# Optimization experiments

Measured on AMD Instinct MI355X. Metric: run time of the kernel, lower is better.

The kernel has to match this reference:

```python
import jax, jax.numpy as jnp
import numpy as np

jax.config.update("jax_enable_x64", True)  # original uses double for Cholesky stability

LAM = 1.0


def _safe_pow(x, a):
    # |x|**a, with a gradient-safe handling of x == 0 (result is 0 for a > 0;
    # naive 0**a has nan grad w.r.t. a via log(0)).
    ax = jnp.abs(x)
    safe = jnp.where(ax == 0, 1.0, ax)
    return jnp.where(ax == 0, 0.0, safe ** a)


def _dx_cov(alpha, tau, T):
    # fGn (increment) covariance; stationary -> depends only on lag k = j - i (Toeplitz)
    t = jnp.arange(T - 1, dtype=jnp.float64)
    DT = (t[None, :] - t[:, None])[None, :, :]          # [1, T-1, T-1]
    a = alpha[:, None, None].astype(jnp.float64)        # [BS, 1, 1]
    tb = tau[:, None, None].astype(jnp.float64)
    R = 0.5 * (_safe_pow(DT + 1.0, a) + _safe_pow(DT - 1.0, a) - 2.0 * _safe_pow(DT, a))
    adt = jnp.abs(DT)
    # exponential taper beyond lag tau; clamp exponent so unused branch can't overflow
    decay = jnp.exp(-LAM * jnp.maximum(adt - tb, 0.0))
    R = jnp.where(adt >= tb, R * decay, R)
    return R                                            # [BS, T-1, T-1] float64


def setup_inputs() -> dict:
    key = jax.random.key(0)
    k1, k2, k3, k4 = jax.random.split(key, 4)
    BS, T, dim = 64, 1024, 3
    alpha = (0.5 + jax.random.uniform(k1, (BS,))).astype(jnp.float32)        # (0.5, 1.5) valid fBM exponent
    tau = (20.0 + 50.0 * jax.random.uniform(k2, (BS,))).astype(jnp.float32)  # taper lag > 0
    diffusion = (0.5 + jax.random.uniform(k3, (BS,))).astype(jnp.float32)
    du = jax.random.normal(k4, (BS, T - 1, dim), dtype=jnp.float32)          # hoisted torch.randn
    return {"alpha": alpha, "tau": tau, "diffusion": diffusion, "du": du, "T": T}


def reference(alpha, tau, diffusion, du, T):
    BS, dim = alpha.shape[0], du.shape[-1]
    C = _dx_cov(alpha, tau, T)                           # [BS, T-1, T-1] float64
    L = jnp.linalg.cholesky(C).astype(jnp.float32)       # batched Cholesky, cast like torch
    du_s = du * jnp.sqrt(diffusion)[:, None, None]       # scale noise by sqrt(D)
    dx = L @ du_s                                        # [BS, T-1, dim]
    x = jnp.cumsum(dx, axis=1)
    zeros = jnp.zeros((BS, 1, dim), dtype=x.dtype)
    return jnp.concatenate([zeros, x], axis=1)           # [BS, T, dim]
```

## Files before the change

### kernel.cpp

```cpp
#include <hip/hip_runtime.h>
#include <math.h>


#define TM1 1023
#define NTH 1024
#define K0  128
#define CSTRIDE 129

__device__ __forceinline__ float bperm(int a, float v) {
    return __int_as_float(__builtin_amdgcn_ds_bpermute(a, __float_as_int(v)));
}
__device__ __forceinline__ float rdlane(float v, int s) {
    return __int_as_float(__builtin_amdgcn_readlane(__float_as_int(v), s));
}
__device__ __forceinline__ float dpp_shl1(float v) {
    return __int_as_float(__builtin_amdgcn_update_dpp(
        0, __float_as_int(v), 0x130, 0xF, 0xF, true));
}
__device__ __forceinline__ int uslot(int k) { return ((k & 3) << 8) | (k >> 2); }

__device__ __forceinline__ float4 ldus(const float4* us4s, int k) {
    int kc = (k < 0) ? 0 : k;
    float4 v = us4s[uslot(kc)];
    if (k < 0) { v.x = 0.f; v.y = 0.f; v.z = 0.f; }
    return v;
}

template<bool MIXED>
__device__ __forceinline__ void conv_quad(
    const float4* us4s, const float* colDT, float lca, float lcb,
    int B, int jq, int quad, float4* ypx4, float4* ypy4, float4* ypz4)
{
    const int   j0   = jq << 5;
    const float lsel = (jq < 2) ? lca : lcb;

    float4 q0 = MIXED ? ldus(us4s, B + 0 - j0) : us4s[uslot(B + 0 - j0)];
    float4 q1 = MIXED ? ldus(us4s, B + 1 - j0) : us4s[uslot(B + 1 - j0)];
    float4 q2 = MIXED ? ldus(us4s, B + 2 - j0) : us4s[uslot(B + 2 - j0)];
    float4 q3 = MIXED ? ldus(us4s, B + 3 - j0) : us4s[uslot(B + 3 - j0)];

    float a0x=0,a0y=0,a0z=0, a1x=0,a1y=0,a1z=0;
    float a2x=0,a2y=0,a2z=0, a3x=0,a3y=0,a3z=0;

    #pragma unroll 8
    for (int jj = 0; jj < 32; ++jj) {
        const int j = j0 + jj;
        float lcj = rdlane(lsel, j & 63);
        float c0 = lcj, c1 = lcj, c2 = lcj, c3 = lcj;
        if (MIXED) {
            int p = B - j;
            float4 h = *reinterpret_cast<const float4*>(&colDT[(j << 7) + B]);
            c0 = (p + 0 < 128) ? h.x : lcj;
            c1 = (p + 1 < 128) ? h.y : lcj;
            c2 = (p + 2 < 128) ? h.z : lcj;
            c3 = (p + 3 < 128) ? h.w : lcj;
        }
        a0x = fmaf(c0, q0.x, a0x); a0y = fmaf(c0, q0.y, a0y); a0z = fmaf(c0, q0.z, a0z);
        a1x = fmaf(c1, q1.x, a1x); a1y = fmaf(c1, q1.y, a1y); a1z = fmaf(c1, q1.z, a1z);
        a2x = fmaf(c2, q2.x, a2x); a2y = fmaf(c2, q2.y, a2y); a2z = fmaf(c2, q2.z, a2z);
        a3x = fmaf(c3, q3.x, a3x); a3y = fmaf(c3, q3.y, a3y); a3z = fmaf(c3, q3.z, a3z);
        int xi = B - j - 1;
        float4 nv = MIXED ? ldus(us4s, xi) : us4s[uslot(xi)];
        q3 = q2; q2 = q1; q1 = q0; q0 = nv;
    }
    ypx4[(jq << 8) + quad] = make_float4(a0x, a1x, a2x, a3x);
    ypy4[(jq << 8) + quad] = make_float4(a0y, a1y, a2y, a3y);
    ypz4[(jq << 8) + quad] = make_float4(a0z, a1z, a2z, a3z);
}

__global__ __launch_bounds__(NTH, 1)
void fbm_schur_kernel(const float* __restrict__ alpha,
                      const float* __restrict__ tau,
                      const float* __restrict__ diffusion,
                      const float* __restrict__ du,
                      float* __restrict__ out)
{
    const int b   = blockIdx.x;
    const int tid = threadIdx.x;
    const int w   = tid >> 6;
    const int l   = tid & 63;

    __shared__ float  colDT[K0 * CSTRIDE];
    __shared__ float4 us4[1024];
    __shared__ float4 ypx4[4 * 256];
    __shared__ float4 ypy4[4 * 256];
    __shared__ float4 ypz4[4 * 256];
    __shared__ float  Lc[128];
    __shared__ float  wtot[48];

    const float sd = sqrtf(diffusion[b]);
    const float* dub = du + (size_t)b * (TM1 * 3);

    if (w > 0) {
        for (int e = tid - 64; e < TM1 * 3; e += (NTH - 64)) {
            int k = e / 3, d = e - 3 * k;
            ((float*)&us4[uslot(k)])[d] = dub[e] * sd;
        }
        for (int i = tid - 64; i < K0; i += (NTH - 64))
            colDT[i * CSTRIDE + 128] = 0.f;
        if (tid == 64) us4[uslot(1023)] = make_float4(0.f, 0.f, 0.f, 0.f);
    } else {
        const double a  = (double)alpha[b];
        const double tb = (double)tau[b];
        auto cov = [&](int k) -> float {
            if (k == 0) return 1.0f;
            double dk = (double)k;
            double ck = 0.5 * (pow(dk + 1.0, a) + pow(dk - 1.0, a) - 2.0 * pow(dk, a));
            if (dk >= tb) ck *= exp(tb - dk);
            return (float)ck;
        };
        float g1a = cov(l);
        float g1b = cov(l + 64);
        float g2a = (l == 0) ? 0.f : g1a;
        float g2b = g1b;

        int probe = __builtin_amdgcn_update_dpp(0, l + 100, 0x130, 0xF, 0xF, true);
        const bool dpp_ok = (__builtin_amdgcn_readlane(probe, 5) == 106);
        const int addr_up = ((l + 1) & 63) << 2;

#define SCHUR_LOOP(SHA, SHB)                                               \
        for (int k = 0; k < K0; ++k) {                                     \
            float den  = rdlane(g1a, 0);                                   \
            float sc   = __frsqrt_rn(den);                                 \
            colDT[l * CSTRIDE + k]        = g1a * sc;                      \
            colDT[(64 + l) * CSTRIDE + k] = g1b * sc;                      \
            float num  = rdlane(g2a, 1);                                   \
            float r    = num * __builtin_amdgcn_rcpf(den);                 \
            float wrap = rdlane(g2b, 0);                                   \
            float g2pa = (SHA);                                            \
            float g2pb = (SHB);                                            \
            if (l == 63) { g2pa = wrap; g2pb = 0.f; }                      \
            float n1a = fmaf(-r, g2pa, g1a);                               \
            float n1b = fmaf(-r, g2pb, g1b);                               \
            g2a = fmaf(-r, g1a, g2pa);                                     \
            g2b = fmaf(-r, g1b, g2pb);                                     \
            g1a = n1a; g1b = n1b;                                          \
        }
        if (dpp_ok) {
            SCHUR_LOOP(dpp_shl1(g2a), dpp_shl1(g2b))
        } else {
            SCHUR_LOOP(bperm(addr_up, g2a), bperm(addr_up, g2b))
        }
#undef SCHUR_LOOP
        float sc = __frsqrt_rn(rdlane(g1a, 0));
        Lc[l]      = g1a * sc;
        Lc[64 + l] = g1b * sc;
    }
    __syncthreads();

    {
        float lca = Lc[l], lcb = Lc[64 + l];
        const int jq   = w & 3;
        const int rb   = w >> 2;
        const int quad = (rb << 6) + l;
        const int B    = quad << 2;
        if (rb == 0)
            conv_quad<true >(us4, colDT, lca, lcb, B, jq, quad, ypx4, ypy4, ypz4);
        else
            conv_quad<false>(us4, colDT, lca, lcb, B, jq, quad, ypx4, ypy4, ypz4);
    }
    __syncthreads();

    const int i = tid;
    float sx = 0.f, sy = 0.f, sz = 0.f;
    if (i < TM1) {
        const float* px = (const float*)ypx4;
        const float* py = (const float*)ypy4;
        const float* pz = (const float*)ypz4;
        sx = px[i] + px[1024 + i] + px[2048 + i] + px[3072 + i];
        sy = py[i] + py[1024 + i] + py[2048 + i] + py[3072 + i];
        sz = pz[i] + pz[1024 + i] + pz[2048 + i] + pz[3072 + i];
    }
    #pragma unroll
    for (int off = 1; off < 64; off <<= 1) {
        float tx = __shfl_up(sx, off);
        float ty = __shfl_up(sy, off);
        float tz = __shfl_up(sz, off);
        if (l >= off) { sx += tx; sy += ty; sz += tz; }
    }
    if (l == 63) { wtot[w * 3 + 0] = sx; wtot[w * 3 + 1] = sy; wtot[w * 3 + 2] = sz; }
    __syncthreads();

    float ox = 0.f, oy = 0.f, oz = 0.f;
    for (int q = 0; q < w; ++q) {
        ox += wtot[q * 3 + 0]; oy += wtot[q * 3 + 1]; oz += wtot[q * 3 + 2];
    }
    float* outb = out + (size_t)b * (TM1 + 1) * 3;
    if (i < TM1) {
        outb[(i + 1) * 3 + 0] = sx + ox;
        outb[(i + 1) * 3 + 1] = sy + oy;
        outb[(i + 1) * 3 + 2] = sz + oz;
    }
    if (tid == 0) { outb[0] = 0.f; outb[1] = 0.f; outb[2] = 0.f; }
}

extern "C" void kernel_launch(void* const* d_in, const int* in_sizes, int n_in,
                              void* d_out, int out_size, void* d_ws, size_t ws_size,
                              hipStream_t stream)
{
    const float* alpha     = (const float*)d_in[0];
    const float* tau       = (const float*)d_in[1];
    const float* diffusion = (const float*)d_in[2];
    const float* du        = (const float*)d_in[3];
    float* out = (float*)d_out;
    const int BS = in_sizes[0];

    fbm_schur_kernel<<<dim3(BS), dim3(NTH), 0, stream>>>(
        alpha, tau, diffusion, du, out);
}
```

Before: 76.50 us.

## Truncate Schur recursion by tau, reuse pow values, track pivot, DPP scan

Limits the Schur/Levinson recursion to K = min(128, ceil(tau)+48) steps, relying on the exponential taper so later columns equal the stationary limit column. Cuts the number of double pow calls by computing one pow per lag and sharing neighbours through shuffles. Updates the pivot algebraically instead of reading it with readlane, which shortens the serial dependency chain. Replaces the shuffle-based wave prefix scan with a DPP scan guarded by a runtime check. Truncating at K is an approximation whose accuracy depends on tau and the 48-lag margin.

```diff
diff --git a/kernel.cpp b/kernel.cpp
--- a/kernel.cpp
+++ b/kernel.cpp
@@ -16,6 +16,21 @@
 __device__ __forceinline__ float dpp_shl1(float v) {
     return __int_as_float(__builtin_amdgcn_update_dpp(
         0, __float_as_int(v), 0x130, 0xF, 0xF, true));
+}
+template<int CTRL, int RM, bool BC>
+__device__ __forceinline__ float dppadd(float s) {
+    float t = __int_as_float(__builtin_amdgcn_update_dpp(
+        0, __float_as_int(s), CTRL, RM, 0xF, BC));
+    return s + t;
+}
+__device__ __forceinline__ float dpp_scan(float s) {
+    s = dppadd<0x111, 0xF, true >(s);
+    s = dppadd<0x112, 0xF, true >(s);
+    s = dppadd<0x114, 0xF, true >(s);
+    s = dppadd<0x118, 0xF, true >(s);
+    s = dppadd<0x142, 0xA, false>(s);
+    s = dppadd<0x143, 0xC, false>(s);
+    return s;
 }
 __device__ __forceinline__ int uslot(int k) { return ((k & 3) << 8) | (k >> 2); }
 
@@ -29,10 +44,11 @@
 template<bool MIXED>
 __device__ __forceinline__ void conv_quad(
     const float4* us4s, const float* colDT, float lca, float lcb,
-    int B, int jq, int quad, float4* ypx4, float4* ypy4, float4* ypz4)
+    int B, int jq, int quad, int K, float4* ypx4, float4* ypy4, float4* ypz4)
 {
-    const int   j0   = jq << 5;
-    const float lsel = (jq < 2) ? lca : lcb;
+    const int      j0   = jq << 5;
+    const float    lsel = (jq < 2) ? lca : lcb;
+    const unsigned Ku   = (unsigned)K;
 
     float4 q0 = MIXED ? ldus(us4s, B + 0 - j0) : us4s[uslot(B + 0 - j0)];
     float4 q1 = MIXED ? ldus(us4s, B + 1 - j0) : us4s[uslot(B + 1 - j0)];
@@ -50,10 +66,10 @@
         if (MIXED) {
             int p = B - j;
             float4 h = *reinterpret_cast<const float4*>(&colDT[(j << 7) + B]);
-            c0 = (p + 0 < 128) ? h.x : lcj;
-            c1 = (p + 1 < 128) ? h.y : lcj;
-            c2 = (p + 2 < 128) ? h.z : lcj;
-            c3 = (p + 3 < 128) ? h.w : lcj;
+            c0 = ((unsigned)(p + 0) < Ku) ? h.x : lcj;
+            c1 = ((unsigned)(p + 1) < Ku) ? h.y : lcj;
+            c2 = ((unsigned)(p + 2) < Ku) ? h.z : lcj;
+            c3 = ((unsigned)(p + 3) < Ku) ? h.w : lcj;
         }
         a0x = fmaf(c0, q0.x, a0x); a0y = fmaf(c0, q0.y, a0y); a0z = fmaf(c0, q0.z, a0z);
         a1x = fmaf(c1, q1.x, a1x); a1y = fmaf(c1, q1.y, a1y); a1z = fmaf(c1, q1.z, a1z);
@@ -89,6 +105,8 @@
     __shared__ float  wtot[48];
 
     const float sd = sqrtf(diffusion[b]);
+    const float tv = tau[b];
+    const int   K  = min(K0, (int)ceilf(tv) + 48);
     const float* dub = du + (size_t)b * (TM1 * 3);
 
     if (w > 0) {
@@ -101,16 +119,29 @@
         if (tid == 64) us4[uslot(1023)] = make_float4(0.f, 0.f, 0.f, 0.f);
     } else {
         const double a  = (double)alpha[b];
-        const double tb = (double)tau[b];
-        auto cov = [&](int k) -> float {
+        const double tb = (double)tv;
+        double pa = pow((double)(l == 0 ? 128 : l), a);
+        double pb = pow((double)(l + 64), a);
+        double pam1 = __shfl_up(pa, 1);
+        double pap1 = __shfl_down(pa, 1);
+        double pbm1 = __shfl_up(pb, 1);
+        double pbp1 = __shfl_down(pb, 1);
+        double p63  = __shfl(pa, 63);
+        double p64  = __shfl(pb, 0);
+        double p128 = __shfl(pa, 0);
+        if (l == 1)  pam1 = 0.0;
+        if (l == 63) pap1 = p64;
+        if (l == 0)  pbm1 = p63;
+        if (l == 63) pbp1 = p128;
+        auto covk = [&](int k, double pm, double p0, double pp) -> float {
             if (k == 0) return 1.0f;
+            double ck = 0.5 * (pp + pm - 2.0 * p0);
             double dk = (double)k;
-            double ck = 0.5 * (pow(dk + 1.0, a) + pow(dk - 1.0, a) - 2.0 * pow(dk, a));
             if (dk >= tb) ck *= exp(tb - dk);
             return (float)ck;
         };
-        float g1a = cov(l);
-        float g1b = cov(l + 64);
+        float g1a = covk(l,      pam1, (l == 0 ? 0.0 : pa), pap1);
+        float g1b = covk(l + 64, pbm1, pb,                  pbp1);
         float g2a = (l == 0) ? 0.f : g1a;
         float g2b = g1b;
 
@@ -118,14 +149,13 @@
         const bool dpp_ok = (__builtin_amdgcn_readlane(probe, 5) == 106);
         const int addr_up = ((l + 1) & 63) << 2;
 
+        float den = 1.0f, rcpden = 1.0f, sc = 1.0f;
 #define SCHUR_LOOP(SHA, SHB)                                               \
-        for (int k = 0; k < K0; ++k) {                                     \
-            float den  = rdlane(g1a, 0);                                   \
-            float sc   = __frsqrt_rn(den);                                 \
+        for (int k = 0; k < K; ++k) {                                      \
             colDT[l * CSTRIDE + k]        = g1a * sc;                      \
             colDT[(64 + l) * CSTRIDE + k] = g1b * sc;                      \
             float num  = rdlane(g2a, 1);                                   \
-            float r    = num * __builtin_amdgcn_rcpf(den);                 \
+            float r    = num * rcpden;                                     \
             float wrap = rdlane(g2b, 0);                                   \
             float g2pa = (SHA);                                            \
             float g2pb = (SHB);                                            \
@@ -135,6 +165,9 @@
             g2a = fmaf(-r, g1a, g2pa);                                     \
             g2b = fmaf(-r, g1b, g2pb);                                     \
             g1a = n1a; g1b = n1b;                                          \
+            den    = fmaf(-r, num, den);                                   \
+            rcpden = __builtin_amdgcn_rcpf(den);                           \
+            sc     = __frsqrt_rn(den);                                     \
         }
         if (dpp_ok) {
             SCHUR_LOOP(dpp_shl1(g2a), dpp_shl1(g2b))
@@ -142,7 +175,6 @@
             SCHUR_LOOP(bperm(addr_up, g2a), bperm(addr_up, g2b))
         }
 #undef SCHUR_LOOP
-        float sc = __frsqrt_rn(rdlane(g1a, 0));
         Lc[l]      = g1a * sc;
         Lc[64 + l] = g1b * sc;
     }
@@ -155,9 +187,9 @@
         const int quad = (rb << 6) + l;
         const int B    = quad << 2;
         if (rb == 0)
-            conv_quad<true >(us4, colDT, lca, lcb, B, jq, quad, ypx4, ypy4, ypz4);
+            conv_quad<true >(us4, colDT, lca, lcb, B, jq, quad, K, ypx4, ypy4, ypz4);
         else
-            conv_quad<false>(us4, colDT, lca, lcb, B, jq, quad, ypx4, ypy4, ypz4);
+            conv_quad<false>(us4, colDT, lca, lcb, B, jq, quad, K, ypx4, ypy4, ypz4);
     }
     __syncthreads();
 
@@ -171,12 +203,20 @@
         sy = py[i] + py[1024 + i] + py[2048 + i] + py[3072 + i];
         sz = pz[i] + pz[1024 + i] + pz[2048 + i] + pz[3072 + i];
     }
-    #pragma unroll
-    for (int off = 1; off < 64; off <<= 1) {
-        float tx = __shfl_up(sx, off);
-        float ty = __shfl_up(sy, off);
-        float tz = __shfl_up(sz, off);
-        if (l >= off) { sx += tx; sy += ty; sz += tz; }
+    {
+        float pv = dpp_scan(1.0f);
+        const bool scan_ok = (rdlane(pv, 63) == 64.0f) && (rdlane(pv, 21) == 22.0f);
+        if (scan_ok) {
+            sx = dpp_scan(sx); sy = dpp_scan(sy); sz = dpp_scan(sz);
+        } else {
+            #pragma unroll
+            for (int off = 1; off < 64; off <<= 1) {
+                float tx = __shfl_up(sx, off);
+                float ty = __shfl_up(sy, off);
+                float tz = __shfl_up(sz, off);
+                if (l >= off) { sx += tx; sy += ty; sz += tz; }
+            }
+        }
     }
     if (l == 63) { wtot[w * 3 + 0] = sx; wtot[w * 3 + 1] = sy; wtot[w * 3 + 2] = sz; }
     __syncthreads();
```

After: 76.39 us. No clear change (-0.1%).
